# Performance work log

Measured on AMD Instinct MI355X. Metric: run time of the kernel, lower is better.

## Reference

```python
import jax, jax.numpy as jnp
import numpy as np

NUM_USERS = 50000
NUM_MOVIES = 20000
NNZ = 2000000
NUM_POS = NNZ // 10
NEG_SAMPLE_SIZE = 5
IN_FEATS = 128
NUM_HIDDEN = 64
BETA = 0.01
GAMMA = 0.01


def setup_inputs() -> dict:
    key = jax.random.key(0)
    ks = jax.random.split(key, 10)
    features = jax.random.normal(ks[0], (NUM_MOVIES, IN_FEATS), dtype=jnp.float32)
    W_enc = jax.random.normal(ks[1], (IN_FEATS, NUM_HIDDEN), dtype=jnp.float32) / np.sqrt(IN_FEATS)
    b_enc = jnp.zeros((NUM_HIDDEN,), dtype=jnp.float32)
    W_p = jax.random.normal(ks[2], (NUM_HIDDEN, NUM_HIDDEN), dtype=jnp.float32) / np.sqrt(NUM_HIDDEN)
    W_q = jax.random.normal(ks[3], (NUM_HIDDEN, NUM_HIDDEN), dtype=jnp.float32) / np.sqrt(NUM_HIDDEN)
    b_u = jnp.zeros((NUM_USERS,), dtype=jnp.float32)
    b_i = jnp.zeros((NUM_MOVIES,), dtype=jnp.float32)
    vals = jax.random.uniform(ks[4], (NNZ,), dtype=jnp.float32) + 0.5  # positive ratings
    rows = jax.random.randint(ks[5], (NNZ,), 0, NUM_USERS, dtype=jnp.int32)
    cols = jax.random.randint(ks[6], (NNZ,), 0, NUM_MOVIES, dtype=jnp.int32)
    pos_idx = jax.random.randint(ks[7], (NUM_POS,), 0, NNZ, dtype=jnp.int32)
    neg_item_idx = jax.random.randint(ks[8], (NUM_POS * NEG_SAMPLE_SIZE,), 0, NUM_MOVIES, dtype=jnp.int32)
    return {
        "features": features, "W_enc": W_enc, "b_enc": b_enc,
        "W_p": W_p, "W_q": W_q, "b_u": b_u, "b_i": b_i,
        "vals": vals, "rows": rows, "cols": cols,
        "pos_idx": pos_idx, "neg_item_idx": neg_item_idx,
        "neg_sample_size": NEG_SAMPLE_SIZE,
    }


def reference(features, W_enc, b_enc, W_p, W_q, b_u, b_i,
              vals, rows, cols, pos_idx, neg_item_idx, neg_sample_size):
    # encode + gconv projections -> item factor matrices P, Q  [M, d]
    h = features @ W_enc + b_enc
    P = h @ W_p
    Q = h @ W_q

    # sparse COO matmul: user_emb_full[u] = sum_{(u,i) in spm} vals * P[i]
    user_emb_full = jax.ops.segment_sum(vals[:, None] * P[cols], rows,
                                        num_segments=NUM_USERS)  # [U, d]
    # user_deg = spm.dot(ones)
    user_deg = jax.ops.segment_sum(vals, rows, num_segments=NUM_USERS)  # [U]

    def est_rating(user_idx, item_idx):
        bu = b_u[user_idx]
        bi = b_i[item_idx]
        ue = user_emb_full[user_idx] / user_deg[user_idx][:, None]
        return bu + bi + jnp.sum(ue * Q[item_idx], axis=1)

    user_idx = rows[pos_idx]
    item_idx = cols[pos_idx]
    r_ui = est_rating(user_idx, item_idx)[:, None]                 # [P, 1]
    neg_user_idx = jnp.repeat(user_idx, neg_sample_size)
    neg_r_ui = est_rating(neg_user_idx, neg_item_idx).reshape(-1, neg_sample_size)  # [P, S]

    diff = 1.0 - (r_ui - neg_r_ui)
    loss = (jnp.sum(diff * diff) * 0.5
            + BETA * 0.5 * jnp.sum(P * P + Q * Q)
            + GAMMA * 0.5 * (jnp.sum(b_u * b_u) + jnp.sum(b_i * b_i)))
    return loss
```

## Files before the change

### kernel.cpp

```cpp
#include <hip/hip_runtime.h>

#define HIDDEN 64
#define BETA 0.01f
#define GAMMA 0.01f

#define BUCKET_SHIFT 7
#define BUCKET_W     (1 << BUCKET_SHIFT)
#define TILE_E       8192

__device__ inline unsigned short f2bf(float f) {
    unsigned x = __float_as_uint(f);
    return (unsigned short)((x + 0x7fffu + ((x >> 16) & 1u)) >> 16);
}
__device__ inline float bf2f(unsigned short b) {
    return __uint_as_float(((unsigned)b) << 16);
}

__global__ void __launch_bounds__(256)
encode_kernel(const float* __restrict__ features,
              const float* __restrict__ W_enc,
              const float* __restrict__ b_enc,
              const float* __restrict__ W_p,
              const float* __restrict__ W_q,
              unsigned short* __restrict__ Ph,
              unsigned short* __restrict__ Qh,
              float* __restrict__ partials, int slot_base,
              int num_movies, int in_feats) {
    __shared__ float hs[16][HIDDEN];
    const int tid = threadIdx.x;
    const int j = tid & 63;
    const int wv = tid >> 6;
    const int m0 = blockIdx.x * 16 + wv * 4;

    const int c0 = min(m0 + 0, num_movies - 1);
    const int c1 = min(m0 + 1, num_movies - 1);
    const int c2 = min(m0 + 2, num_movies - 1);
    const int c3 = min(m0 + 3, num_movies - 1);
    const float* fr0 = features + (size_t)c0 * in_feats;
    const float* fr1 = features + (size_t)c1 * in_feats;
    const float* fr2 = features + (size_t)c2 * in_feats;
    const float* fr3 = features + (size_t)c3 * in_feats;

    float h0 = 0.0f, h1 = 0.0f, h2 = 0.0f, h3 = 0.0f;
    #pragma unroll 4
    for (int f = 0; f < in_feats; f += 4) {
        const float w_a = W_enc[(f + 0) * HIDDEN + j];
        const float w_b = W_enc[(f + 1) * HIDDEN + j];
        const float w_c = W_enc[(f + 2) * HIDDEN + j];
        const float w_d = W_enc[(f + 3) * HIDDEN + j];
        const float4 a0 = *(const float4*)(fr0 + f);
        const float4 a1 = *(const float4*)(fr1 + f);
        const float4 a2 = *(const float4*)(fr2 + f);
        const float4 a3 = *(const float4*)(fr3 + f);
        h0 = fmaf(a0.x, w_a, h0); h0 = fmaf(a0.y, w_b, h0);
        h0 = fmaf(a0.z, w_c, h0); h0 = fmaf(a0.w, w_d, h0);
        h1 = fmaf(a1.x, w_a, h1); h1 = fmaf(a1.y, w_b, h1);
        h1 = fmaf(a1.z, w_c, h1); h1 = fmaf(a1.w, w_d, h1);
        h2 = fmaf(a2.x, w_a, h2); h2 = fmaf(a2.y, w_b, h2);
        h2 = fmaf(a2.z, w_c, h2); h2 = fmaf(a2.w, w_d, h2);
        h3 = fmaf(a3.x, w_a, h3); h3 = fmaf(a3.y, w_b, h3);
        h3 = fmaf(a3.z, w_c, h3); h3 = fmaf(a3.w, w_d, h3);
    }
    const float be = b_enc[j];
    hs[wv * 4 + 0][j] = h0 + be;
    hs[wv * 4 + 1][j] = h1 + be;
    hs[wv * 4 + 2][j] = h2 + be;
    hs[wv * 4 + 3][j] = h3 + be;
    __syncthreads();

    float p0 = 0.0f, p1 = 0.0f, p2 = 0.0f, p3 = 0.0f;
    float q0 = 0.0f, q1 = 0.0f, q2 = 0.0f, q3 = 0.0f;
    #pragma unroll 4
    for (int f = 0; f < HIDDEN; f += 4) {
        const float wp0 = W_p[(f + 0) * HIDDEN + j];
        const float wp1 = W_p[(f + 1) * HIDDEN + j];
        const float wp2 = W_p[(f + 2) * HIDDEN + j];
        const float wp3 = W_p[(f + 3) * HIDDEN + j];
        const float wq0 = W_q[(f + 0) * HIDDEN + j];
        const float wq1 = W_q[(f + 1) * HIDDEN + j];
        const float wq2 = W_q[(f + 2) * HIDDEN + j];
        const float wq3 = W_q[(f + 3) * HIDDEN + j];
        const float4 v0 = *(const float4*)(&hs[wv * 4 + 0][f]);
        const float4 v1 = *(const float4*)(&hs[wv * 4 + 1][f]);
        const float4 v2 = *(const float4*)(&hs[wv * 4 + 2][f]);
        const float4 v3 = *(const float4*)(&hs[wv * 4 + 3][f]);
        p0 = fmaf(v0.x, wp0, p0); p0 = fmaf(v0.y, wp1, p0);
        p0 = fmaf(v0.z, wp2, p0); p0 = fmaf(v0.w, wp3, p0);
        q0 = fmaf(v0.x, wq0, q0); q0 = fmaf(v0.y, wq1, q0);
        q0 = fmaf(v0.z, wq2, q0); q0 = fmaf(v0.w, wq3, q0);
        p1 = fmaf(v1.x, wp0, p1); p1 = fmaf(v1.y, wp1, p1);
        p1 = fmaf(v1.z, wp2, p1); p1 = fmaf(v1.w, wp3, p1);
        q1 = fmaf(v1.x, wq0, q1); q1 = fmaf(v1.y, wq1, q1);
        q1 = fmaf(v1.z, wq2, q1); q1 = fmaf(v1.w, wq3, q1);
        p2 = fmaf(v2.x, wp0, p2); p2 = fmaf(v2.y, wp1, p2);
        p2 = fmaf(v2.z, wp2, p2); p2 = fmaf(v2.w, wp3, p2);
        q2 = fmaf(v2.x, wq0, q2); q2 = fmaf(v2.y, wq1, q2);
        q2 = fmaf(v2.z, wq2, q2); q2 = fmaf(v2.w, wq3, q2);
        p3 = fmaf(v3.x, wp0, p3); p3 = fmaf(v3.y, wp1, p3);
        p3 = fmaf(v3.z, wp2, p3); p3 = fmaf(v3.w, wp3, p3);
        q3 = fmaf(v3.x, wq0, q3); q3 = fmaf(v3.y, wq1, q3);
        q3 = fmaf(v3.z, wq2, q3); q3 = fmaf(v3.w, wq3, q3);
    }

    float reg = 0.0f;
    if (m0 + 0 < num_movies) {
        Ph[(size_t)(m0 + 0) * HIDDEN + j] = f2bf(p0);
        Qh[(size_t)(m0 + 0) * HIDDEN + j] = f2bf(q0);
        reg += p0 * p0 + q0 * q0;
    }
    if (m0 + 1 < num_movies) {
        Ph[(size_t)(m0 + 1) * HIDDEN + j] = f2bf(p1);
        Qh[(size_t)(m0 + 1) * HIDDEN + j] = f2bf(q1);
        reg += p1 * p1 + q1 * q1;
    }
    if (m0 + 2 < num_movies) {
        Ph[(size_t)(m0 + 2) * HIDDEN + j] = f2bf(p2);
        Qh[(size_t)(m0 + 2) * HIDDEN + j] = f2bf(q2);
        reg += p2 * p2 + q2 * q2;
    }
    if (m0 + 3 < num_movies) {
        Ph[(size_t)(m0 + 3) * HIDDEN + j] = f2bf(p3);
        Qh[(size_t)(m0 + 3) * HIDDEN + j] = f2bf(q3);
        reg += p3 * p3 + q3 * q3;
    }

    for (int off = 32; off; off >>= 1) reg += __shfl_down(reg, off);
    __shared__ float s_part[4];
    if (j == 0) s_part[wv] = reg;
    __syncthreads();
    if (tid == 0) {
        float t = (s_part[0] + s_part[1]) + (s_part[2] + s_part[3]);
        partials[slot_base + blockIdx.x] = 0.5f * BETA * t;
    }
}

__global__ void tilehist_kernel(const int* __restrict__ rows, int nnz,
                                int nbuckets, int ntiles,
                                unsigned* __restrict__ tileHist) {
    extern __shared__ unsigned hist[];
    const int t = blockIdx.x;
    const int tid = threadIdx.x;
    for (int i = tid; i < nbuckets; i += blockDim.x) hist[i] = 0;
    __syncthreads();

    const int base = t * TILE_E;
    const int kmax = TILE_E / 256;
    for (int k = 0; k < kmax; ++k) {
        const int e = base + k * 256 + tid;
        if (e < nnz) atomicAdd(&hist[rows[e] >> BUCKET_SHIFT], 1u);
    }
    __syncthreads();
    for (int i = tid; i < nbuckets; i += blockDim.x)
        tileHist[(size_t)i * ntiles + t] = hist[i];
}

__global__ void chunksum_kernel(const unsigned* __restrict__ src, int n,
                                unsigned* __restrict__ sums) {
    __shared__ unsigned s[256];
    const int t = threadIdx.x;
    const int i = blockIdx.x * 256 + t;
    s[t] = (i < n) ? src[i] : 0u;
    __syncthreads();
    for (int off = 128; off; off >>= 1) {
        if (t < off) s[t] += s[t + off];
        __syncthreads();
    }
    if (t == 0) sums[blockIdx.x] = s[0];
}

__global__ void __launch_bounds__(512)
scantop_kernel(const unsigned* __restrict__ sums, int nchunks,
               unsigned* __restrict__ chunk_off,
               unsigned* __restrict__ offs, int n, int total) {
    __shared__ unsigned s[512];
    const int t = threadIdx.x;
    unsigned x = (t < nchunks) ? sums[t] : 0u;
    s[t] = x;
    __syncthreads();
    for (int off = 1; off < 512; off <<= 1) {
        unsigned v = (t >= off) ? s[t - off] : 0u;
        __syncthreads();
        s[t] += v;
        __syncthreads();
    }
    if (t < nchunks) chunk_off[t] = s[t] - x;
    if (t == 0) offs[n] = (unsigned)total;
}

__global__ void exscan_kernel(const unsigned* __restrict__ src, int n,
                              const unsigned* __restrict__ chunk_off,
                              unsigned* __restrict__ dst) {
    __shared__ unsigned s[256];
    const int t = threadIdx.x;
    const int i = blockIdx.x * 256 + t;
    unsigned x = (i < n) ? src[i] : 0u;
    s[t] = x;
    __syncthreads();
    for (int off = 1; off < 256; off <<= 1) {
        unsigned v = (t >= off) ? s[t - off] : 0u;
        __syncthreads();
        s[t] += v;
        __syncthreads();
    }
    if (i < n) dst[i] = chunk_off[blockIdx.x] + s[t] - x;
}

__global__ void partition_kernel(const int* __restrict__ rows,
                                 const int* __restrict__ cols,
                                 const float* __restrict__ vals, int nnz,
                                 int nbuckets, int ntiles,
                                 const unsigned* __restrict__ offsB,
                                 uint2* __restrict__ temp,
                                 unsigned char* __restrict__ lu8) {
    extern __shared__ unsigned smem[];
    unsigned* hist = smem;
    unsigned* lofs = smem + nbuckets;
    const int t = blockIdx.x;
    const int tid = threadIdx.x;
    for (int i = tid; i < nbuckets; i += blockDim.x) {
        hist[i] = 0;
        lofs[i] = offsB[(size_t)i * ntiles + t];
    }
    __syncthreads();

    const int base = t * TILE_E;
    const int kmax = TILE_E / 256;
    for (int k = 0; k < kmax; ++k) {
        const int e = base + k * 256 + tid;
        if (e < nnz) {
            const int r = rows[e];
            const int b = r >> BUCKET_SHIFT;
            const unsigned lrank = atomicAdd(&hist[b], 1u);
            const unsigned dst = lofs[b] + lrank;
            const unsigned key = ((unsigned)r << 15) | (unsigned)cols[e];
            temp[dst] = make_uint2(key, __float_as_uint(vals[e]));
            lu8[dst] = (unsigned char)(r & (BUCKET_W - 1));
        }
    }
}

__global__ void __launch_bounds__(512)
csr_scatter_kernel(const uint2* __restrict__ temp,
                   const unsigned char* __restrict__ lu8,
                   const unsigned* __restrict__ offsB,
                   int* __restrict__ row_start,
                   uint2* __restrict__ pairs,
                   int ntiles, int num_users, int nbB) {
    __shared__ int cnt[BUCKET_W];
    __shared__ int scan_s[BUCKET_W];
    __shared__ int cur[BUCKET_W];
    const int b = blockIdx.x;
    const int tid = threadIdx.x;
    const int ubase = b << BUCKET_SHIFT;
    const int s0 = (int)offsB[(size_t)b * ntiles];
    const int s1 = (int)offsB[(size_t)(b + 1) * ntiles];

    if (tid < BUCKET_W) cnt[tid] = 0;
    __syncthreads();
    for (int s = s0 + tid; s < s1; s += 512)
        atomicAdd(&cnt[lu8[s]], 1);
    __syncthreads();

    int x = 0;
    if (tid < BUCKET_W) {
        x = cnt[tid];
        scan_s[tid] = x;
    }
    __syncthreads();
    for (int off = 1; off < BUCKET_W; off <<= 1) {
        int v = 0;
        if (tid < BUCKET_W && tid >= off) v = scan_s[tid - off];
        __syncthreads();
        if (tid < BUCKET_W) scan_s[tid] += v;
        __syncthreads();
    }
    if (tid < BUCKET_W) {
        const int start = s0 + scan_s[tid] - x;
        cur[tid] = start;
        if (ubase + tid < num_users) row_start[ubase + tid] = start;
    }
    if (b == nbB - 1 && tid == 0) row_start[num_users] = s1;
    __syncthreads();

    for (int s = s0 + tid; s < s1; s += 512) {
        const uint2 e = temp[s];
        const int lu = (int)(e.x >> 15) - ubase;
        const int dst = atomicAdd(&cur[lu], 1);
        pairs[dst] = make_uint2(e.x & 0x7fffu, e.y);
    }
}

__global__ void gather_kernel(const int* __restrict__ row_start,
                              const uint2* __restrict__ pairs,
                              const unsigned short* __restrict__ Ph,
                              float* __restrict__ user_emb,
                              float* __restrict__ user_deg, int nu) {
    const int lane = threadIdx.x & 63;
    const int half = lane >> 5;
    const int hl = lane & 31;
    const int u = (blockIdx.x * blockDim.x + threadIdx.x) >> 6;
    if (u >= nu) return;

    const int s0 = row_start[u];
    const int s1 = row_start[u + 1];
    float ax0 = 0.0f, ay0 = 0.0f, ax1 = 0.0f, ay1 = 0.0f;
    float ax2 = 0.0f, ay2 = 0.0f, ax3 = 0.0f, ay3 = 0.0f;
    float deg = 0.0f;
    int s = s0;
    for (; s + 7 < s1; s += 8) {
        const uint2 p0 = pairs[s + half];
        const uint2 p1 = pairs[s + 2 + half];
        const uint2 p2 = pairs[s + 4 + half];
        const uint2 p3 = pairs[s + 6 + half];
        const unsigned w0 = *(const unsigned*)(Ph + (size_t)p0.x * HIDDEN + 2 * hl);
        const unsigned w1 = *(const unsigned*)(Ph + (size_t)p1.x * HIDDEN + 2 * hl);
        const unsigned w2 = *(const unsigned*)(Ph + (size_t)p2.x * HIDDEN + 2 * hl);
        const unsigned w3 = *(const unsigned*)(Ph + (size_t)p3.x * HIDDEN + 2 * hl);
        const float v0 = __uint_as_float(p0.y);
        const float v1 = __uint_as_float(p1.y);
        const float v2 = __uint_as_float(p2.y);
        const float v3 = __uint_as_float(p3.y);
        ax0 = fmaf(v0, __uint_as_float(w0 << 16), ax0);
        ay0 = fmaf(v0, __uint_as_float(w0 & 0xffff0000u), ay0);
        ax1 = fmaf(v1, __uint_as_float(w1 << 16), ax1);
        ay1 = fmaf(v1, __uint_as_float(w1 & 0xffff0000u), ay1);
        ax2 = fmaf(v2, __uint_as_float(w2 << 16), ax2);
        ay2 = fmaf(v2, __uint_as_float(w2 & 0xffff0000u), ay2);
        ax3 = fmaf(v3, __uint_as_float(w3 << 16), ax3);
        ay3 = fmaf(v3, __uint_as_float(w3 & 0xffff0000u), ay3);
        deg += (v0 + v1) + (v2 + v3);
    }
    for (; s + 1 < s1; s += 2) {
        const uint2 pr = pairs[s + half];
        const float v = __uint_as_float(pr.y);
        const unsigned w = *(const unsigned*)(Ph + (size_t)pr.x * HIDDEN + 2 * hl);
        ax0 = fmaf(v, __uint_as_float(w << 16), ax0);
        ay0 = fmaf(v, __uint_as_float(w & 0xffff0000u), ay0);
        deg += v;
    }
    if (s < s1 && half == 0) {
        const uint2 pr = pairs[s];
        const float v = __uint_as_float(pr.y);
        const unsigned w = *(const unsigned*)(Ph + (size_t)pr.x * HIDDEN + 2 * hl);
        ax0 = fmaf(v, __uint_as_float(w << 16), ax0);
        ay0 = fmaf(v, __uint_as_float(w & 0xffff0000u), ay0);
        deg += v;
    }

    float xv = (ax0 + ax1) + (ax2 + ax3);
    float yv = (ay0 + ay1) + (ay2 + ay3);
    xv += __shfl_xor(xv, 32);
    yv += __shfl_xor(yv, 32);
    deg += __shfl_xor(deg, 32);
    if (half == 0) {
        *(float2*)(user_emb + (size_t)u * HIDDEN + 2 * hl) =
            make_float2(xv, yv);
        if (hl == 0) user_deg[u] = deg;
    }
}

__device__ inline float dot16(const uint4* __restrict__ q,
                              const float* __restrict__ ue) {
    float d = 0.0f;
    #pragma unroll
    for (int h = 0; h < 2; ++h) {
        const uint4 v = q[h];
        const unsigned w0 = v.x, w1 = v.y, w2 = v.z, w3 = v.w;
        d = fmaf(ue[h * 8 + 0], __uint_as_float(w0 << 16), d);
        d = fmaf(ue[h * 8 + 1], __uint_as_float(w0 & 0xffff0000u), d);
        d = fmaf(ue[h * 8 + 2], __uint_as_float(w1 << 16), d);
        d = fmaf(ue[h * 8 + 3], __uint_as_float(w1 & 0xffff0000u), d);
        d = fmaf(ue[h * 8 + 4], __uint_as_float(w2 << 16), d);
        d = fmaf(ue[h * 8 + 5], __uint_as_float(w2 & 0xffff0000u), d);
        d = fmaf(ue[h * 8 + 6], __uint_as_float(w3 << 16), d);
        d = fmaf(ue[h * 8 + 7], __uint_as_float(w3 & 0xffff0000u), d);
    }
    return d;
}

template <int S>
__global__ void loss4_kernel(const float* __restrict__ user_emb,
                             const float* __restrict__ user_deg,
                             const unsigned short* __restrict__ Qh,
                             const float* __restrict__ b_u,
                             const float* __restrict__ b_i,
                             const int* __restrict__ rows,
                             const int* __restrict__ cols,
                             const int* __restrict__ pos_idx,
                             const int* __restrict__ neg_item_idx,
                             int num_pos,
                             float* __restrict__ partials, int slot_base) {
    const int tid = blockIdx.x * blockDim.x + threadIdx.x;
    const int g = tid >> 2;
    const int l = tid & 3;
    float acc = 0.0f;

    if (g < num_pos) {
        const int e = pos_idx[g];
        const int u = rows[e];
        const int ii = cols[e];
        const float invdeg = 1.0f / user_deg[u];

        float ue[16];
        {
            const float4* uep =
                (const float4*)(user_emb + (size_t)u * HIDDEN + l * 16);
            #pragma unroll
            for (int k = 0; k < 4; ++k) {
                const float4 t4 = uep[k];
                ue[4 * k + 0] = t4.x * invdeg;
                ue[4 * k + 1] = t4.y * invdeg;
                ue[4 * k + 2] = t4.z * invdeg;
                ue[4 * k + 3] = t4.w * invdeg;
            }
        }

        int jarr[S];
        float part[1 + S];
        part[0] = dot16((const uint4*)(Qh + (size_t)ii * HIDDEN + l * 16), ue);
        #pragma unroll
        for (int s = 0; s < S; ++s) {
            const int j = neg_item_idx[(size_t)g * S + s];
            jarr[s] = j;
            part[1 + s] =
                dot16((const uint4*)(Qh + (size_t)j * HIDDEN + l * 16), ue);
        }

        #pragma unroll
        for (int k = 0; k < 1 + S; ++k) {
            part[k] += __shfl_xor(part[k], 1);
            part[k] += __shfl_xor(part[k], 2);
        }

        if (l == 0) {
            const float bu = b_u[u];
            const float r = bu + b_i[ii] + part[0];
            #pragma unroll
            for (int s = 0; s < S; ++s) {
                const float nr = bu + b_i[jarr[s]] + part[1 + s];
                const float diff = 1.0f - (r - nr);
                acc += 0.5f * diff * diff;
            }
        }
    }

    for (int off = 32; off; off >>= 1) acc += __shfl_down(acc, off);
    __shared__ float s_part[16];
    const int wave = threadIdx.x >> 6;
    const int lane = threadIdx.x & 63;
    if (lane == 0) s_part[wave] = acc;
    __syncthreads();
    if (threadIdx.x == 0) {
        float t = 0.0f;
        const int nw = blockDim.x >> 6;
        for (int w = 0; w < nw; ++w) t += s_part[w];
        partials[slot_base + blockIdx.x] = t;
    }
}

__global__ void loss_generic_kernel(const float* __restrict__ user_emb,
                                    const float* __restrict__ user_deg,
                                    const unsigned short* __restrict__ Qh,
                                    const float* __restrict__ b_u,
                                    const float* __restrict__ b_i,
                                    const int* __restrict__ rows,
                                    const int* __restrict__ cols,
                                    const int* __restrict__ pos_idx,
                                    const int* __restrict__ neg_item_idx,
                                    int num_pos, int S,
                                    float* __restrict__ partials,
                                    int slot_base) {
    const int p = blockIdx.x * blockDim.x + threadIdx.x;
    float acc = 0.0f;
    if (p < num_pos) {
        const int e = pos_idx[p];
        const int u = rows[e];
        const int ii = cols[e];
        const float invdeg = 1.0f / user_deg[u];
        float ue[HIDDEN];
        #pragma unroll
        for (int kk = 0; kk < HIDDEN; ++kk)
            ue[kk] = user_emb[(size_t)u * HIDDEN + kk] * invdeg;
        const float bu = b_u[u];
        float dot = 0.0f;
        #pragma unroll
        for (int kk = 0; kk < HIDDEN; ++kk)
            dot = fmaf(ue[kk], bf2f(Qh[(size_t)ii * HIDDEN + kk]), dot);
        const float rr = bu + b_i[ii] + dot;
        for (int s = 0; s < S; ++s) {
            const int j = neg_item_idx[(size_t)p * S + s];
            float dn = 0.0f;
            #pragma unroll
            for (int kk = 0; kk < HIDDEN; ++kk)
                dn = fmaf(ue[kk], bf2f(Qh[(size_t)j * HIDDEN + kk]), dn);
            const float nr = bu + b_i[j] + dn;
            const float diff = 1.0f - (rr - nr);
            acc += 0.5f * diff * diff;
        }
    }
    for (int off = 32; off; off >>= 1) acc += __shfl_down(acc, off);
    __shared__ float s_part[16];
    const int wave = threadIdx.x >> 6;
    const int lane = threadIdx.x & 63;
    if (lane == 0) s_part[wave] = acc;
    __syncthreads();
    if (threadIdx.x == 0) {
        float t = 0.0f;
        const int nw = blockDim.x >> 6;
        for (int w = 0; w < nw; ++w) t += s_part[w];
        partials[slot_base + blockIdx.x] = t;
    }
}

__global__ void bias_reg_kernel(const float* __restrict__ b_u, int nu,
                                const float* __restrict__ b_i, int ni,
                                float* __restrict__ partials, int slot_base) {
    const int tid = blockIdx.x * blockDim.x + threadIdx.x;
    const int stride = gridDim.x * blockDim.x;
    const int n = nu + ni;
    float acc = 0.0f;
    for (int x = tid; x < n; x += stride) {
        float v = (x < nu) ? b_u[x] : b_i[x - nu];
        acc += v * v;
    }
    for (int off = 32; off; off >>= 1) acc += __shfl_down(acc, off);
    __shared__ float s_part[16];
    const int wave = threadIdx.x >> 6;
    const int lane = threadIdx.x & 63;
    if (lane == 0) s_part[wave] = acc;
    __syncthreads();
    if (threadIdx.x == 0) {
        float t = 0.0f;
        const int nw = blockDim.x >> 6;
        for (int w = 0; w < nw; ++w) t += s_part[w];
        partials[slot_base + blockIdx.x] = 0.5f * GAMMA * t;
    }
}

__global__ void final_reduce_kernel(const float* __restrict__ partials, int n,
                                    float* __restrict__ out) {
    __shared__ float s[256];
    float a = 0.0f;
    for (int i = threadIdx.x; i < n; i += 256) a += partials[i];
    s[threadIdx.x] = a;
    __syncthreads();
    for (int off = 128; off; off >>= 1) {
        if (threadIdx.x < off) s[threadIdx.x] += s[threadIdx.x + off];
        __syncthreads();
    }
    if (threadIdx.x == 0) out[0] = s[0];
}

extern "C" void kernel_launch(void* const* d_in, const int* in_sizes, int n_in,
                              void* d_out, int out_size, void* d_ws, size_t ws_size,
                              hipStream_t stream) {
    const float* features     = (const float*)d_in[0];
    const float* W_enc        = (const float*)d_in[1];
    const float* b_enc        = (const float*)d_in[2];
    const float* W_p          = (const float*)d_in[3];
    const float* W_q          = (const float*)d_in[4];
    const float* b_u          = (const float*)d_in[5];
    const float* b_i          = (const float*)d_in[6];
    const float* vals         = (const float*)d_in[7];
    const int*   rows         = (const int*)d_in[8];
    const int*   cols         = (const int*)d_in[9];
    const int*   pos_idx      = (const int*)d_in[10];
    const int*   neg_item_idx = (const int*)d_in[11];

    const int num_users  = in_sizes[5];
    const int num_movies = in_sizes[6];
    const int in_feats   = in_sizes[0] / num_movies;
    const int nnz        = in_sizes[7];
    const int num_pos    = in_sizes[10];
    const int S          = in_sizes[11] / num_pos;

    const int nbB    = (num_users + BUCKET_W - 1) >> BUCKET_SHIFT;
    const int ntiles = (nnz + TILE_E - 1) / TILE_E;
    const int scanNB = nbB * ntiles;
    const int n1b    = (scanNB + 255) / 256;

    const int enc_blocks  = (num_movies + 15) / 16;
    const int loss_blocks = (S == 5) ? (int)(((size_t)num_pos * 4 + 255) / 256)
                                     : (num_pos + 255) / 256;
    const int bias_blocks = 128;
    const int slot_pq   = 0;
    const int slot_loss = enc_blocks;
    const int slot_bias = enc_blocks + loss_blocks;
    const int n_slots   = slot_bias + bias_blocks;

    auto align256 = [](size_t x) { return (x + 255) & ~(size_t)255; };
    char* ws = (char*)d_ws;
    size_t off = 0;
    unsigned short* Ph = (unsigned short*)(ws + off);
    off += align256((size_t)num_movies * HIDDEN * 2);
    unsigned short* Qh = (unsigned short*)(ws + off);
    off += align256((size_t)num_movies * HIDDEN * 2);
    char* U = ws + off;
    const size_t emb_bytes = align256((size_t)num_users * HIDDEN * 4);
    const size_t tmp_bytes = align256((size_t)nnz * 8);
    uint2* temp     = (uint2*)U;
    float* user_emb = (float*)U;
    off += (emb_bytes > tmp_bytes) ? emb_bytes : tmp_bytes;
    float* user_deg = (float*)(ws + off); off += align256((size_t)num_users * 4);
    int*   row_start= (int*)(ws + off);   off += align256((size_t)(num_users + 1) * 4);
    unsigned* tileHistB = (unsigned*)(ws + off); off += align256((size_t)scanNB * 4);
    unsigned* offsB     = (unsigned*)(ws + off); off += align256((size_t)(scanNB + 1) * 4);
    unsigned* sums_b    = (unsigned*)(ws + off); off += align256(512 * 4);
    unsigned* top_b     = (unsigned*)(ws + off); off += align256(512 * 4);
    uint2* pairs        = (uint2*)(ws + off);    off += align256((size_t)nnz * 8);
    unsigned char* lu8  = (unsigned char*)(ws + off); off += align256((size_t)nnz);
    float* partials     = (float*)(ws + off);    off += align256((size_t)n_slots * 4);

    float* out = (float*)d_out;

    encode_kernel<<<enc_blocks, 256, 0, stream>>>(
        features, W_enc, b_enc, W_p, W_q, Ph, Qh, partials, slot_pq,
        num_movies, in_feats);

    tilehist_kernel<<<ntiles, 256, (size_t)nbB * 4, stream>>>(
        rows, nnz, nbB, ntiles, tileHistB);
    chunksum_kernel<<<n1b, 256, 0, stream>>>(tileHistB, scanNB, sums_b);
    scantop_kernel<<<1, 512, 0, stream>>>(sums_b, n1b, top_b, offsB, scanNB, nnz);
    exscan_kernel<<<n1b, 256, 0, stream>>>(tileHistB, scanNB, top_b, offsB);

    partition_kernel<<<ntiles, 256, (size_t)nbB * 8, stream>>>(
        rows, cols, vals, nnz, nbB, ntiles, offsB, temp, lu8);
    csr_scatter_kernel<<<nbB, 512, 0, stream>>>(temp, lu8, offsB, row_start,
                                                pairs, ntiles, num_users, nbB);

    gather_kernel<<<(num_users * 64 + 255) / 256, 256, 0, stream>>>(
        row_start, pairs, Ph, user_emb, user_deg, num_users);

    if (S == 5) {
        loss4_kernel<5><<<loss_blocks, 256, 0, stream>>>(
            user_emb, user_deg, Qh, b_u, b_i, rows, cols, pos_idx,
            neg_item_idx, num_pos, partials, slot_loss);
    } else {
        loss_generic_kernel<<<loss_blocks, 256, 0, stream>>>(
            user_emb, user_deg, Qh, b_u, b_i, rows, cols, pos_idx,
            neg_item_idx, num_pos, S, partials, slot_loss);
    }

    bias_reg_kernel<<<bias_blocks, 256, 0, stream>>>(b_u, num_users,
                                                     b_i, num_movies,
                                                     partials, slot_bias);

    final_reduce_kernel<<<1, 256, 0, stream>>>(partials, n_slots, out);
}
```

Measured before the change: 191.0 us.

## Drop lu8 side array, widen user buckets, use nontemporal loads in CSR build

```diff
diff --git a/kernel.cpp b/kernel.cpp
--- a/kernel.cpp
+++ b/kernel.cpp
@@ -4,7 +4,7 @@
 #define BETA 0.01f
 #define GAMMA 0.01f
 
-#define BUCKET_SHIFT 7
+#define BUCKET_SHIFT 8
 #define BUCKET_W     (1 << BUCKET_SHIFT)
 #define TILE_E       8192
 
@@ -147,7 +147,10 @@
     const int kmax = TILE_E / 256;
     for (int k = 0; k < kmax; ++k) {
         const int e = base + k * 256 + tid;
-        if (e < nnz) atomicAdd(&hist[rows[e] >> BUCKET_SHIFT], 1u);
+        if (e < nnz) {
+            const int r = __builtin_nontemporal_load(rows + e);
+            atomicAdd(&hist[r >> BUCKET_SHIFT], 1u);
+        }
     }
     __syncthreads();
     for (int i = tid; i < nbuckets; i += blockDim.x)
@@ -210,8 +213,7 @@
                                  const float* __restrict__ vals, int nnz,
                                  int nbuckets, int ntiles,
                                  const unsigned* __restrict__ offsB,
-                                 uint2* __restrict__ temp,
-                                 unsigned char* __restrict__ lu8) {
+                                 uint2* __restrict__ temp) {
     extern __shared__ unsigned smem[];
     unsigned* hist = smem;
     unsigned* lofs = smem + nbuckets;
@@ -228,20 +230,20 @@
     for (int k = 0; k < kmax; ++k) {
         const int e = base + k * 256 + tid;
         if (e < nnz) {
-            const int r = rows[e];
+            const int r = __builtin_nontemporal_load(rows + e);
+            const int c = __builtin_nontemporal_load(cols + e);
+            const float v = __builtin_nontemporal_load(vals + e);
             const int b = r >> BUCKET_SHIFT;
             const unsigned lrank = atomicAdd(&hist[b], 1u);
             const unsigned dst = lofs[b] + lrank;
-            const unsigned key = ((unsigned)r << 15) | (unsigned)cols[e];
-            temp[dst] = make_uint2(key, __float_as_uint(vals[e]));
-            lu8[dst] = (unsigned char)(r & (BUCKET_W - 1));
+            const unsigned key = ((unsigned)r << 15) | (unsigned)c;
+            temp[dst] = make_uint2(key, __float_as_uint(v));
         }
     }
 }
 
-__global__ void __launch_bounds__(512)
+__global__ void __launch_bounds__(1024)
 csr_scatter_kernel(const uint2* __restrict__ temp,
-                   const unsigned char* __restrict__ lu8,
                    const unsigned* __restrict__ offsB,
                    int* __restrict__ row_start,
                    uint2* __restrict__ pairs,
@@ -257,8 +259,11 @@
 
     if (tid < BUCKET_W) cnt[tid] = 0;
     __syncthreads();
-    for (int s = s0 + tid; s < s1; s += 512)
-        atomicAdd(&cnt[lu8[s]], 1);
+    const unsigned* tx = (const unsigned*)temp;
+    for (int s = s0 + tid; s < s1; s += 1024) {
+        const unsigned key = __builtin_nontemporal_load(tx + 2 * (size_t)s);
+        atomicAdd(&cnt[(int)(key >> 15) - ubase], 1);
+    }
     __syncthreads();
 
     int x = 0;
@@ -282,11 +287,14 @@
     if (b == nbB - 1 && tid == 0) row_start[num_users] = s1;
     __syncthreads();
 
-    for (int s = s0 + tid; s < s1; s += 512) {
-        const uint2 e = temp[s];
-        const int lu = (int)(e.x >> 15) - ubase;
+    for (int s = s0 + tid; s < s1; s += 1024) {
+        const unsigned long long ev = __builtin_nontemporal_load(
+            (const unsigned long long*)temp + s);
+        const unsigned ex = (unsigned)ev;
+        const unsigned ey = (unsigned)(ev >> 32);
+        const int lu = (int)(ex >> 15) - ubase;
         const int dst = atomicAdd(&cur[lu], 1);
-        pairs[dst] = make_uint2(e.x & 0x7fffu, e.y);
+        pairs[dst] = make_uint2(ex & 0x7fffu, ey);
     }
 }
 
@@ -608,7 +616,6 @@
     unsigned* sums_b    = (unsigned*)(ws + off); off += align256(512 * 4);
     unsigned* top_b     = (unsigned*)(ws + off); off += align256(512 * 4);
     uint2* pairs        = (uint2*)(ws + off);    off += align256((size_t)nnz * 8);
-    unsigned char* lu8  = (unsigned char*)(ws + off); off += align256((size_t)nnz);
     float* partials     = (float*)(ws + off);    off += align256((size_t)n_slots * 4);
 
     float* out = (float*)d_out;
@@ -624,9 +631,9 @@
     exscan_kernel<<<n1b, 256, 0, stream>>>(tileHistB, scanNB, top_b, offsB);
 
     partition_kernel<<<ntiles, 256, (size_t)nbB * 8, stream>>>(
-        rows, cols, vals, nnz, nbB, ntiles, offsB, temp, lu8);
-    csr_scatter_kernel<<<nbB, 512, 0, stream>>>(temp, lu8, offsB, row_start,
-                                                pairs, ntiles, num_users, nbB);
+        rows, cols, vals, nnz, nbB, ntiles, offsB, temp);
+    csr_scatter_kernel<<<nbB, 1024, 0, stream>>>(temp, offsB, row_start,
+                                                 pairs, ntiles, num_users, nbB);
 
     gather_kernel<<<(num_users * 64 + 255) / 256, 256, 0, stream>>>(
         row_start, pairs, Ph, user_emb, user_deg, num_users);
```

After: 187.7 us. Within noise of the previous version (-1.7%).
